# Kernel tuning notes

Measured on AMD Instinct MI355X. Metric: run time of the kernel, lower is better.

Reference implementation:

```python
import jax, jax.numpy as jnp
import numpy as np

HIDDEN = 2048
N_HEADS = 32
N_KV_HEADS = 8
HEAD_DIM = HIDDEN // N_HEADS  # 64
GROUPS = N_HEADS // N_KV_HEADS  # 4
ROPE_BASE = 10000.0


def _rope_cos_sin(seq_len, dim, dtype):
    inv_freq = 1.0 / (ROPE_BASE ** (jnp.arange(0, dim, 2, dtype=jnp.float32) / dim))
    t = jnp.arange(seq_len, dtype=jnp.float32)
    freqs = jnp.outer(t, inv_freq)            # [S, dim/2]
    emb = jnp.concatenate([freqs, freqs], -1)  # [S, dim]
    return jnp.cos(emb).astype(dtype), jnp.sin(emb).astype(dtype)


def _rotate_half(x):
    x1, x2 = jnp.split(x, 2, axis=-1)
    return jnp.concatenate([-x2, x1], axis=-1)


def setup_inputs() -> dict:
    key = jax.random.key(0)
    ks = jax.random.split(key, 5)
    x = jax.random.normal(ks[0], (2, 2048, HIDDEN), dtype=jnp.float32)
    scale = 0.02
    wq = jax.random.normal(ks[1], (HIDDEN, N_HEADS * HEAD_DIM), dtype=jnp.float32) * scale
    wk = jax.random.normal(ks[2], (HIDDEN, N_KV_HEADS * HEAD_DIM), dtype=jnp.float32) * scale
    wv = jax.random.normal(ks[3], (HIDDEN, N_KV_HEADS * HEAD_DIM), dtype=jnp.float32) * scale
    wo = jax.random.normal(ks[4], (N_HEADS * HEAD_DIM, HIDDEN), dtype=jnp.float32) * scale
    return {"x": x, "wq": wq, "wk": wk, "wv": wv, "wo": wo}


def reference(x, wq, wk, wv, wo):
    b, s, _ = x.shape
    # projections (torch Linear with weight stored transposed -> plain matmul here)
    q = (x @ wq).reshape(b, s, N_HEADS, HEAD_DIM).transpose(0, 2, 1, 3)      # [b,nh,s,d]
    k = (x @ wk).reshape(b, s, N_KV_HEADS, HEAD_DIM).transpose(0, 2, 1, 3)   # [b,kvh,s,d]
    v = (x @ wv).reshape(b, s, N_KV_HEADS, HEAD_DIM).transpose(0, 2, 1, 3)   # [b,kvh,s,d]

    cos, sin = _rope_cos_sin(s, HEAD_DIM, x.dtype)  # [s,d]
    cos = cos[None, None]  # [1,1,s,d]
    sin = sin[None, None]
    q = q * cos + _rotate_half(q) * sin
    k = k * cos + _rotate_half(k) * sin

    # GQA: group query heads per KV head instead of expanding K/V
    qg = q.reshape(b, N_KV_HEADS, GROUPS, s, HEAD_DIM)
    scores = jnp.einsum('bhgqd,bhkd->bhgqk', qg, k) / np.sqrt(HEAD_DIM).astype(x.dtype)
    probs = jax.nn.softmax(scores.astype(jnp.float32), axis=-1).astype(x.dtype)
    out = jnp.einsum('bhgqk,bhkd->bhgqd', probs, v)          # [b,kvh,g,s,d]
    out = out.reshape(b, N_HEADS, s, HEAD_DIM).transpose(0, 2, 1, 3).reshape(b, s, HIDDEN)
    return out @ wo
```

## Files before the change

kernel.cpp:

```cpp
#include <hip/hip_runtime.h>


typedef __bf16 bf16;
typedef __bf16 bf16x4_t __attribute__((ext_vector_type(4)));
typedef __bf16 bf16x8_t __attribute__((ext_vector_type(8)));
typedef float  f32x4_t  __attribute__((ext_vector_type(4)));

#define S_LEN 2048
#define HID   2048
#define NH    32
#define KVH   8
#define HD    64

__device__ __forceinline__ void async_copy16(const void* g, void* l) {
  __builtin_amdgcn_global_load_lds(
      (const __attribute__((address_space(1))) void*)g,
      (__attribute__((address_space(3))) void*)l, 16, 0, 0);
}

__global__ __launch_bounds__(256) void cast_bf16_kernel(
    const float* __restrict__ src, bf16* __restrict__ dst) {
  int i = (blockIdx.x * 256 + threadIdx.x) * 4;
  float4 v = *(const float4*)(src + i);
  bf16x4_t o;
  o[0] = (bf16)v.x; o[1] = (bf16)v.y; o[2] = (bf16)v.z; o[3] = (bf16)v.w;
  *(bf16x4_t*)(dst + i) = o;
}

__global__ __launch_bounds__(256) void wtrans_kernel(
    const float* __restrict__ src, bf16* __restrict__ dst, int C, int dstStride) {
  __shared__ float tile[32][33];
  int c0 = blockIdx.x * 32, r0 = blockIdx.y * 32;
  int t = threadIdx.x;
  int r = t >> 3, c4 = (t & 7) * 4;
  float4 v = *(const float4*)(src + (size_t)(r0 + r) * C + c0 + c4);
  tile[r][c4] = v.x; tile[r][c4 + 1] = v.y; tile[r][c4 + 2] = v.z; tile[r][c4 + 3] = v.w;
  __syncthreads();
  int cc = t >> 3, r4 = (t & 7) * 4;
  bf16x4_t o;
  o[0] = (bf16)tile[r4][cc];     o[1] = (bf16)tile[r4 + 1][cc];
  o[2] = (bf16)tile[r4 + 2][cc]; o[3] = (bf16)tile[r4 + 3][cc];
  *(bf16x4_t*)(dst + (size_t)(c0 + cc) * dstStride + r0 + r4) = o;
}

__global__ __launch_bounds__(256, 2) void qkv_gemm_rope(
    const bf16* __restrict__ A, const bf16* __restrict__ Bt,
    bf16* __restrict__ q_r, bf16* __restrict__ k_r, bf16* __restrict__ v_t) {
  __shared__ char smem[32768];
  char* As = smem;
  char* Bs = smem + 16384;
  const int tid  = threadIdx.x;
  const int wid  = tid >> 6;
  const int lane = tid & 63;
  const int l15  = lane & 15;
  const int quad = lane >> 4;
  const int wm = wid >> 1, wn = wid & 1;
  const int bm = blockIdx.y * 128;
  const int bn = blockIdx.x * 128;
  const int K = 2048;

  f32x4_t acc[4][4] = {};

  for (int k0 = 0; k0 < K; k0 += 64) {
#pragma unroll
    for (int it = 0; it < 4; ++it) {
      int p = it * 256 + tid;
      int row = p >> 3;
      int j = (p & 7) ^ (row & 7);
      async_copy16(A + (size_t)(bm + row) * K + k0 + j * 8,
                   As + (size_t)(it * 256 + wid * 64) * 16);
      async_copy16(Bt + (size_t)(bn + row) * K + k0 + j * 8,
                   Bs + (size_t)(it * 256 + wid * 64) * 16);
    }
    __syncthreads();
#pragma unroll
    for (int kk = 0; kk < 64; kk += 32) {
      bf16x8_t af[4], bfr[4];
      int cbase = (kk >> 3) + quad;
#pragma unroll
      for (int mt = 0; mt < 4; ++mt) {
        int row = wm * 64 + mt * 16 + l15;
        af[mt] = *(const bf16x8_t*)(As + (size_t)(row * 8 + (cbase ^ (row & 7))) * 16);
      }
#pragma unroll
      for (int nt = 0; nt < 4; ++nt) {
        int row = wn * 64 + nt * 16 + l15;
        bfr[nt] = *(const bf16x8_t*)(Bs + (size_t)(row * 8 + (cbase ^ (row & 7))) * 16);
      }
#pragma unroll
      for (int mt = 0; mt < 4; ++mt)
#pragma unroll
        for (int nt = 0; nt < 4; ++nt)
          acc[mt][nt] = __builtin_amdgcn_mfma_f32_16x16x32_bf16(
              af[mt], bfr[nt], acc[mt][nt], 0, 0, 0);
    }
    __syncthreads();
  }

  const int cb = blockIdx.x * 2 + wn;
  const int rowbase = bm + wm * 64;
  const int bidx = bm >> 11;
  const float LE = 0.41524101186098285f;
  const float SC = 0.18033688011112043f;

  if (cb < 40) {
    const bool isQ = (cb < 32);
    const float sc = isQ ? SC : 1.0f;
    bf16* base = isQ ? (q_r + (size_t)(bidx * NH + cb) * S_LEN * HD)
                     : (k_r + (size_t)(bidx * KVH + (cb - 32)) * S_LEN * HD);
#pragma unroll
    for (int nt = 0; nt < 2; ++nt) {
      int i = nt * 16 + l15;
      float inv = __builtin_exp2f(-(float)i * LE);
#pragma unroll
      for (int mt = 0; mt < 4; ++mt)
#pragma unroll
        for (int r = 0; r < 4; ++r) {
          int row = rowbase + mt * 16 + quad * 4 + r;
          int s = row & 2047;
          float ang = (float)s * inv;
          float sv, cv;
          __sincosf(ang, &sv, &cv);
          float x1 = acc[mt][nt][r], x2 = acc[mt][nt + 2][r];
          bf16* d = base + (size_t)s * HD;
          d[i]      = (bf16)((x1 * cv - x2 * sv) * sc);
          d[i + 32] = (bf16)((x2 * cv + x1 * sv) * sc);
        }
    }
  } else {
    const int kvh = cb - 40;
    bf16* base = v_t + (size_t)(bidx * KVH + kvh) * HD * S_LEN;
#pragma unroll
    for (int nt = 0; nt < 4; ++nt) {
      int d = nt * 16 + l15;
#pragma unroll
      for (int mt = 0; mt < 4; ++mt) {
        int s0 = (rowbase + mt * 16 + quad * 4) & 2047;
        bf16x4_t o;
        o[0] = (bf16)acc[mt][nt][0]; o[1] = (bf16)acc[mt][nt][1];
        o[2] = (bf16)acc[mt][nt][2]; o[3] = (bf16)acc[mt][nt][3];
        *(bf16x4_t*)(base + (size_t)d * S_LEN + s0) = o;
      }
    }
  }
}

template <typename OutT>
__global__ __launch_bounds__(256, 2) void gemm_bt(
    const bf16* __restrict__ A, const bf16* __restrict__ Bt,
    OutT* __restrict__ C, int N, int K) {
  __shared__ char smem[32768];
  char* As = smem;
  char* Bs = smem + 16384;
  const int tid  = threadIdx.x;
  const int wid  = tid >> 6;
  const int lane = tid & 63;
  const int l15  = lane & 15;
  const int quad = lane >> 4;
  const int wm = wid >> 1, wn = wid & 1;
  const int bm = blockIdx.y * 128;
  const int bn = blockIdx.x * 128;

  f32x4_t acc[4][4] = {};

  for (int k0 = 0; k0 < K; k0 += 64) {
#pragma unroll
    for (int it = 0; it < 4; ++it) {
      int p = it * 256 + tid;
      int row = p >> 3;
      int j = (p & 7) ^ (row & 7);
      async_copy16(A + (size_t)(bm + row) * K + k0 + j * 8,
                   As + (size_t)(it * 256 + wid * 64) * 16);
      async_copy16(Bt + (size_t)(bn + row) * K + k0 + j * 8,
                   Bs + (size_t)(it * 256 + wid * 64) * 16);
    }
    __syncthreads();
#pragma unroll
    for (int kk = 0; kk < 64; kk += 32) {
      bf16x8_t af[4], bfr[4];
      int cbase = (kk >> 3) + quad;
#pragma unroll
      for (int mt = 0; mt < 4; ++mt) {
        int row = wm * 64 + mt * 16 + l15;
        af[mt] = *(const bf16x8_t*)(As + (size_t)(row * 8 + (cbase ^ (row & 7))) * 16);
      }
#pragma unroll
      for (int nt = 0; nt < 4; ++nt) {
        int row = wn * 64 + nt * 16 + l15;
        bfr[nt] = *(const bf16x8_t*)(Bs + (size_t)(row * 8 + (cbase ^ (row & 7))) * 16);
      }
#pragma unroll
      for (int mt = 0; mt < 4; ++mt)
#pragma unroll
        for (int nt = 0; nt < 4; ++nt)
          acc[mt][nt] = __builtin_amdgcn_mfma_f32_16x16x32_bf16(
              af[mt], bfr[nt], acc[mt][nt], 0, 0, 0);
    }
    __syncthreads();
  }
#pragma unroll
  for (int mt = 0; mt < 4; ++mt)
#pragma unroll
    for (int nt = 0; nt < 4; ++nt)
#pragma unroll
      for (int r = 0; r < 4; ++r) {
        int row = bm + wm * 64 + mt * 16 + quad * 4 + r;
        int col = bn + wn * 64 + nt * 16 + l15;
        C[(size_t)row * N + col] = (OutT)acc[mt][nt][r];
      }
}

__global__ __launch_bounds__(256, 3) void attn_kernel(
    const bf16* __restrict__ q_r, const bf16* __restrict__ k_r,
    const bf16* __restrict__ v_t, bf16* __restrict__ attn) {
  __shared__ char smem[49152];
  char* Ks = smem;
  char* Vs = smem + 16384;
  char* Ps = smem + 32768;
  const int tid = threadIdx.x;
  const int wid = tid >> 6;
  const int lane = tid & 63;
  const int l15 = lane & 15, quad = lane >> 4;
  const int qh = quad >> 1, ql = quad & 1;
  const int blky = blockIdx.y;
  const int b = blky >> 3, kvh = blky & 7;
  const int h = kvh * 4 + wid;
  const int q0 = blockIdx.x * 32;
  char* Pw = Ps + wid * 4096;

  const bf16* Kg = k_r + (size_t)blky * S_LEN * HD;
  const bf16* Vg = v_t + (size_t)blky * HD * S_LEN;

  bf16x8_t qf0[2], qf1[2];
#pragma unroll
  for (int qt = 0; qt < 2; ++qt) {
    const bf16* qb = q_r + ((size_t)(b * NH + h) * S_LEN + q0 + qt * 16 + l15) * HD;
    qf0[qt] = *(const bf16x8_t*)(qb + quad * 8);
    qf1[qt] = *(const bf16x8_t*)(qb + 32 + quad * 8);
  }
  bf16x8_t ones;
#pragma unroll
  for (int e = 0; e < 8; ++e) ones[e] = (bf16)1.0f;

  f32x4_t o_acc[2][4] = {};
  f32x4_t l_acc[2] = {};

#pragma unroll
  for (int it = 0; it < 4; ++it) {
    int p = it * 256 + tid;
    int row = p >> 3, j = (p & 7) ^ (row & 7);
    async_copy16(Kg + (size_t)row * HD + j * 8,
                 Ks + (size_t)(it * 256 + wid * 64) * 16);
  }

  for (int kt = 0; kt < S_LEN / 128; ++kt) {
    __syncthreads();
#pragma unroll
    for (int it = 0; it < 4; ++it) {
      int p = it * 256 + tid;
      int vrow = p >> 4, vj = (p & 15) ^ (vrow & 15);
      async_copy16(Vg + (size_t)vrow * S_LEN + kt * 128 + vj * 8,
                   Vs + (size_t)(it * 256 + wid * 64) * 16);
    }

    f32x4_t sa[2][8];
#pragma unroll
    for (int t = 0; t < 8; ++t) { sa[0][t] = f32x4_t{0.f,0.f,0.f,0.f}; sa[1][t] = f32x4_t{0.f,0.f,0.f,0.f}; }
#pragma unroll
    for (int t = 0; t < 8; ++t) {
      int row = t * 16 + l15;
      int s3 = l15 & 7;
      bf16x8_t kf0 = *(const bf16x8_t*)(Ks + (size_t)(row * 8 + (quad ^ s3)) * 16);
      bf16x8_t kf1 = *(const bf16x8_t*)(Ks + (size_t)(row * 8 + ((4 + quad) ^ s3)) * 16);
      sa[0][t] = __builtin_amdgcn_mfma_f32_16x16x32_bf16(kf0, qf0[0], sa[0][t], 0, 0, 0);
      sa[0][t] = __builtin_amdgcn_mfma_f32_16x16x32_bf16(kf1, qf1[0], sa[0][t], 0, 0, 0);
      sa[1][t] = __builtin_amdgcn_mfma_f32_16x16x32_bf16(kf0, qf0[1], sa[1][t], 0, 0, 0);
      sa[1][t] = __builtin_amdgcn_mfma_f32_16x16x32_bf16(kf1, qf1[1], sa[1][t], 0, 0, 0);
    }
    __syncthreads();

    if (kt < S_LEN / 128 - 1) {
#pragma unroll
      for (int it = 0; it < 4; ++it) {
        int p = it * 256 + tid;
        int row = p >> 3, j = (p & 7) ^ (row & 7);
        async_copy16(Kg + (size_t)((kt + 1) * 128 + row) * HD + j * 8,
                     Ks + (size_t)(it * 256 + wid * 64) * 16);
      }
    }

#pragma unroll
    for (int qt = 0; qt < 2; ++qt) {
#pragma unroll
      for (int t = 0; t < 8; ++t) {
        bf16x4_t pk;
        pk[0] = (bf16)__builtin_exp2f(sa[qt][t][0]);
        pk[1] = (bf16)__builtin_exp2f(sa[qt][t][1]);
        pk[2] = (bf16)__builtin_exp2f(sa[qt][t][2]);
        pk[3] = (bf16)__builtin_exp2f(sa[qt][t][3]);
        *(bf16x4_t*)(Pw + l15 * 256 + (((2 * t + qh) ^ l15) * 16) + ql * 8) = pk;
      }
#pragma unroll
      for (int c = 0; c < 4; ++c) {
        bf16x8_t pf = *(const bf16x8_t*)(Pw + l15 * 256 + (((4 * c + quad) ^ l15) * 16));
        l_acc[qt] = __builtin_amdgcn_mfma_f32_16x16x32_bf16(ones, pf, l_acc[qt], 0, 0, 0);
#pragma unroll
        for (int nt = 0; nt < 4; ++nt) {
          int d = nt * 16 + l15;
          bf16x8_t vf = *(const bf16x8_t*)(Vs + d * 256 + (((4 * c + quad) ^ l15) * 16));
          o_acc[qt][nt] = __builtin_amdgcn_mfma_f32_16x16x32_bf16(vf, pf, o_acc[qt][nt], 0, 0, 0);
        }
      }
    }
  }

#pragma unroll
  for (int qt = 0; qt < 2; ++qt) {
    float inv = 1.0f / l_acc[qt][0];
#pragma unroll
    for (int nt = 0; nt < 4; ++nt) {
      bf16x4_t o;
      o[0] = (bf16)(o_acc[qt][nt][0] * inv);
      o[1] = (bf16)(o_acc[qt][nt][1] * inv);
      o[2] = (bf16)(o_acc[qt][nt][2] * inv);
      o[3] = (bf16)(o_acc[qt][nt][3] * inv);
      *(bf16x4_t*)(Pw + l15 * 144 + (nt * 16 + quad * 4) * 2) = o;
    }
    int row = lane >> 2, cc = lane & 3;
    bf16x8_t r0 = *(const bf16x8_t*)(Pw + row * 144 + cc * 32);
    bf16x8_t r1 = *(const bf16x8_t*)(Pw + row * 144 + cc * 32 + 16);
    int token = q0 + qt * 16 + row;
    bf16* dst = attn + ((size_t)(b * S_LEN + token)) * HID + h * 64 + cc * 16;
    *(bf16x8_t*)dst = r0;
    *(bf16x8_t*)(dst + 8) = r1;
  }
}

extern "C" void kernel_launch(void* const* d_in, const int* in_sizes, int n_in,
                              void* d_out, int out_size, void* d_ws, size_t ws_size,
                              hipStream_t stream) {
  const float* x  = (const float*)d_in[0];
  const float* wq = (const float*)d_in[1];
  const float* wk = (const float*)d_in[2];
  const float* wv = (const float*)d_in[3];
  const float* wo = (const float*)d_in[4];
  float* out = (float*)d_out;
  char* ws = (char*)d_ws;

  bf16* q_r    = (bf16*)(ws + 0);
  bf16* k_r    = (bf16*)(ws + 16777216);
  bf16* v_t    = (bf16*)(ws + 20971520);
  bf16* wqkv_t = (bf16*)(ws + 25165824);
  bf16* attn   = (bf16*)(ws + 25165824);
  bf16* wo_t   = (bf16*)(ws + 16777216);
  bf16* x_b    = (bf16*)d_out;

  cast_bf16_kernel<<<8192, 256, 0, stream>>>(x, x_b);
  wtrans_kernel<<<dim3(64, 64), 256, 0, stream>>>(wq, wqkv_t, 2048, 2048);
  wtrans_kernel<<<dim3(16, 64), 256, 0, stream>>>(wk, wqkv_t + (size_t)2048 * 2048, 512, 2048);
  wtrans_kernel<<<dim3(16, 64), 256, 0, stream>>>(wv, wqkv_t + (size_t)2560 * 2048, 512, 2048);

  qkv_gemm_rope<<<dim3(24, 32), 256, 0, stream>>>(x_b, wqkv_t, q_r, k_r, v_t);
  attn_kernel<<<dim3(64, 16), 256, 0, stream>>>(q_r, k_r, v_t, attn);

  wtrans_kernel<<<dim3(64, 64), 256, 0, stream>>>(wo, wo_t, 2048, 2048);
  gemm_bt<float><<<dim3(16, 32), 256, 0, stream>>>(attn, wo_t, out, 2048, 2048);
}
```

Before: 356.4 us.

## Read K directly from global, drop K LDS tile, raise attention occupancy

```diff
diff --git a/kernel.cpp b/kernel.cpp
--- a/kernel.cpp
+++ b/kernel.cpp
@@ -210,21 +210,20 @@
       }
 }
 
-__global__ __launch_bounds__(256, 3) void attn_kernel(
+__global__ __launch_bounds__(256, 4) void attn_kernel(
     const bf16* __restrict__ q_r, const bf16* __restrict__ k_r,
     const bf16* __restrict__ v_t, bf16* __restrict__ attn) {
-  __shared__ char smem[49152];
-  char* Ks = smem;
-  char* Vs = smem + 16384;
-  char* Ps = smem + 32768;
+  __shared__ char smem[32768];
+  char* Vs = smem;
+  char* Ps = smem + 16384;
   const int tid = threadIdx.x;
   const int wid = tid >> 6;
   const int lane = tid & 63;
   const int l15 = lane & 15, quad = lane >> 4;
   const int qh = quad >> 1, ql = quad & 1;
   const int blky = blockIdx.y;
-  const int b = blky >> 3, kvh = blky & 7;
-  const int h = kvh * 4 + wid;
+  const int b = blky >> 3;
+  const int h = (blky & 7) * 4 + wid;
   const int q0 = blockIdx.x * 32;
   char* Pw = Ps + wid * 4096;
 
@@ -248,34 +247,63 @@
 #pragma unroll
   for (int it = 0; it < 4; ++it) {
     int p = it * 256 + tid;
-    int row = p >> 3, j = (p & 7) ^ (row & 7);
-    async_copy16(Kg + (size_t)row * HD + j * 8,
-                 Ks + (size_t)(it * 256 + wid * 64) * 16);
+    int vrow = p >> 4, vj = (p & 15) ^ (vrow & 15);
+    async_copy16(Vg + (size_t)vrow * S_LEN + vj * 8,
+                 Vs + (size_t)(it * 256 + wid * 64) * 16);
   }
 
   for (int kt = 0; kt < S_LEN / 128; ++kt) {
-    __syncthreads();
-#pragma unroll
-    for (int it = 0; it < 4; ++it) {
-      int p = it * 256 + tid;
-      int vrow = p >> 4, vj = (p & 15) ^ (vrow & 15);
-      async_copy16(Vg + (size_t)vrow * S_LEN + kt * 128 + vj * 8,
-                   Vs + (size_t)(it * 256 + wid * 64) * 16);
-    }
-
-    f32x4_t sa[2][8];
-#pragma unroll
-    for (int t = 0; t < 8; ++t) { sa[0][t] = f32x4_t{0.f,0.f,0.f,0.f}; sa[1][t] = f32x4_t{0.f,0.f,0.f,0.f}; }
+    f32x4_t sa1[8];
 #pragma unroll
     for (int t = 0; t < 8; ++t) {
-      int row = t * 16 + l15;
-      int s3 = l15 & 7;
-      bf16x8_t kf0 = *(const bf16x8_t*)(Ks + (size_t)(row * 8 + (quad ^ s3)) * 16);
-      bf16x8_t kf1 = *(const bf16x8_t*)(Ks + (size_t)(row * 8 + ((4 + quad) ^ s3)) * 16);
-      sa[0][t] = __builtin_amdgcn_mfma_f32_16x16x32_bf16(kf0, qf0[0], sa[0][t], 0, 0, 0);
-      sa[0][t] = __builtin_amdgcn_mfma_f32_16x16x32_bf16(kf1, qf1[0], sa[0][t], 0, 0, 0);
-      sa[1][t] = __builtin_amdgcn_mfma_f32_16x16x32_bf16(kf0, qf0[1], sa[1][t], 0, 0, 0);
-      sa[1][t] = __builtin_amdgcn_mfma_f32_16x16x32_bf16(kf1, qf1[1], sa[1][t], 0, 0, 0);
+      const bf16* kb = Kg + (size_t)(kt * 128 + t * 16 + l15) * HD;
+      bf16x8_t kf0 = *(const bf16x8_t*)(kb + quad * 8);
+      bf16x8_t kf1 = *(const bf16x8_t*)(kb + 32 + quad * 8);
+      f32x4_t s0 = {};
+      sa1[t] = f32x4_t{0.f, 0.f, 0.f, 0.f};
+      s0 = __builtin_amdgcn_mfma_f32_16x16x32_bf16(kf0, qf0[0], s0, 0, 0, 0);
+      s0 = __builtin_amdgcn_mfma_f32_16x16x32_bf16(kf1, qf1[0], s0, 0, 0, 0);
+      sa1[t] = __builtin_amdgcn_mfma_f32_16x16x32_bf16(kf0, qf0[1], sa1[t], 0, 0, 0);
+      sa1[t] = __builtin_amdgcn_mfma_f32_16x16x32_bf16(kf1, qf1[1], sa1[t], 0, 0, 0);
+      bf16x4_t pk;
+      pk[0] = (bf16)__builtin_exp2f(s0[0]);
+      pk[1] = (bf16)__builtin_exp2f(s0[1]);
+      pk[2] = (bf16)__builtin_exp2f(s0[2]);
+      pk[3] = (bf16)__builtin_exp2f(s0[3]);
+      *(bf16x4_t*)(Pw + l15 * 256 + (((2 * t + qh) ^ l15) * 16) + ql * 8) = pk;
+    }
+    __syncthreads();
+
+#pragma unroll
+    for (int c = 0; c < 4; ++c) {
+      bf16x8_t pf = *(const bf16x8_t*)(Pw + l15 * 256 + (((4 * c + quad) ^ l15) * 16));
+      l_acc[0] = __builtin_amdgcn_mfma_f32_16x16x32_bf16(ones, pf, l_acc[0], 0, 0, 0);
+#pragma unroll
+      for (int nt = 0; nt < 4; ++nt) {
+        int d = nt * 16 + l15;
+        bf16x8_t vf = *(const bf16x8_t*)(Vs + d * 256 + (((4 * c + quad) ^ l15) * 16));
+        o_acc[0][nt] = __builtin_amdgcn_mfma_f32_16x16x32_bf16(vf, pf, o_acc[0][nt], 0, 0, 0);
+      }
+    }
+#pragma unroll
+    for (int t = 0; t < 8; ++t) {
+      bf16x4_t pk;
+      pk[0] = (bf16)__builtin_exp2f(sa1[t][0]);
+      pk[1] = (bf16)__builtin_exp2f(sa1[t][1]);
+      pk[2] = (bf16)__builtin_exp2f(sa1[t][2]);
+      pk[3] = (bf16)__builtin_exp2f(sa1[t][3]);
+      *(bf16x4_t*)(Pw + l15 * 256 + (((2 * t + qh) ^ l15) * 16) + ql * 8) = pk;
+    }
+#pragma unroll
+    for (int c = 0; c < 4; ++c) {
+      bf16x8_t pf = *(const bf16x8_t*)(Pw + l15 * 256 + (((4 * c + quad) ^ l15) * 16));
+      l_acc[1] = __builtin_amdgcn_mfma_f32_16x16x32_bf16(ones, pf, l_acc[1], 0, 0, 0);
+#pragma unroll
+      for (int nt = 0; nt < 4; ++nt) {
+        int d = nt * 16 + l15;
+        bf16x8_t vf = *(const bf16x8_t*)(Vs + d * 256 + (((4 * c + quad) ^ l15) * 16));
+        o_acc[1][nt] = __builtin_amdgcn_mfma_f32_16x16x32_bf16(vf, pf, o_acc[1][nt], 0, 0, 0);
+      }
     }
     __syncthreads();
 
@@ -283,33 +311,9 @@
 #pragma unroll
       for (int it = 0; it < 4; ++it) {
         int p = it * 256 + tid;
-        int row = p >> 3, j = (p & 7) ^ (row & 7);
-        async_copy16(Kg + (size_t)((kt + 1) * 128 + row) * HD + j * 8,
-                     Ks + (size_t)(it * 256 + wid * 64) * 16);
-      }
-    }
-
-#pragma unroll
-    for (int qt = 0; qt < 2; ++qt) {
-#pragma unroll
-      for (int t = 0; t < 8; ++t) {
-        bf16x4_t pk;
-        pk[0] = (bf16)__builtin_exp2f(sa[qt][t][0]);
-        pk[1] = (bf16)__builtin_exp2f(sa[qt][t][1]);
-        pk[2] = (bf16)__builtin_exp2f(sa[qt][t][2]);
-        pk[3] = (bf16)__builtin_exp2f(sa[qt][t][3]);
-        *(bf16x4_t*)(Pw + l15 * 256 + (((2 * t + qh) ^ l15) * 16) + ql * 8) = pk;
-      }
-#pragma unroll
-      for (int c = 0; c < 4; ++c) {
-        bf16x8_t pf = *(const bf16x8_t*)(Pw + l15 * 256 + (((4 * c + quad) ^ l15) * 16));
-        l_acc[qt] = __builtin_amdgcn_mfma_f32_16x16x32_bf16(ones, pf, l_acc[qt], 0, 0, 0);
-#pragma unroll
-        for (int nt = 0; nt < 4; ++nt) {
-          int d = nt * 16 + l15;
-          bf16x8_t vf = *(const bf16x8_t*)(Vs + d * 256 + (((4 * c + quad) ^ l15) * 16));
-          o_acc[qt][nt] = __builtin_amdgcn_mfma_f32_16x16x32_bf16(vf, pf, o_acc[qt][nt], 0, 0, 0);
-        }
+        int vrow = p >> 4, vj = (p & 15) ^ (vrow & 15);
+        async_copy16(Vg + (size_t)vrow * S_LEN + (kt + 1) * 128 + vj * 8,
+                     Vs + (size_t)(it * 256 + wid * 64) * 16);
       }
     }
   }
```

Measured after the change: 361.0 us. Within noise of the previous version (+1.3%).
